# Performance work log

Measured on AMD Instinct MI355X. Metric: run time of the kernel, lower is better.

Reference implementation:

```python
import jax, jax.numpy as jnp
import numpy as np

B, F0, D = 4096, 39, 16
CIN = [128, 128, 128]


def setup_inputs() -> dict:
    key = jax.random.key(0)
    ks = jax.random.split(key, 4)
    x = jax.random.normal(ks[0], (B, F0, D), dtype=jnp.float32)
    fields = [F0] + CIN
    inp = {"embedded_features": x}
    for i in range(len(CIN)):
        cin = F0 * fields[i]
        cout = fields[i + 1]
        kw = jax.random.fold_in(ks[1], i)
        # Conv1d default init scale ~ 1/sqrt(fan_in)
        inp[f"W{i}"] = jax.random.normal(kw, (cout, cin), dtype=jnp.float32) / np.sqrt(cin)
        inp[f"b{i}"] = jnp.zeros((cout,), dtype=jnp.float32)
    return inp


def _cin_layer(X0, Xi, W, b):
    # Math identical to: outer_product [B,F0,Fi,D] -> reshape [B,F0*Fi,D] -> 1x1 Conv1d.
    # Conv1d(kernel=1) over the flattened F0*Fi channel dim is a contraction over (j,k):
    #   Xn[b,h,d] = sum_{j,k} W[h, j*Fi+k] * X0[b,j,d] * Xi[b,k,d] + b[h]
    H = W.shape[0]
    F0_, Fi = X0.shape[1], Xi.shape[1]
    Wr = W.reshape(H, F0_, Fi)
    return jnp.einsum('hjk,bjd,bkd->bhd', Wr, X0, Xi) + b[None, :, None]


def reference(embedded_features, W0, b0, W1, b1, W2, b2):
    X0 = embedded_features  # [B, F0, D]
    Ws = [(W0, b0), (W1, b1), (W2, b2)]
    Xi = X0
    res = []
    for W, b in Ws:
        Xi = _cin_layer(X0, Xi, W, b)  # [B, H_i, D]
        res.append(Xi.sum(axis=2))     # sum over embedding dim
    return jnp.concatenate(res, axis=1)  # [B, sum(cin_size)]
```

## Files before the change

### kernel.cpp

```cpp
#include <hip/hip_runtime.h>
#include <stdint.h>


#define NB_F0 39
#define NB_H  128
#define NB_B  4096

typedef float f32x4  __attribute__((ext_vector_type(4)));
typedef float f32x16 __attribute__((ext_vector_type(16)));
typedef short s16x8  __attribute__((ext_vector_type(8)));

__device__ __forceinline__ void dma16(const void* g, void* l) {
  __builtin_amdgcn_global_load_lds(
      (const __attribute__((address_space(1))) unsigned int*)g,
      (__attribute__((address_space(3))) unsigned int*)l, 16, 0, 0);
}

__device__ __forceinline__ unsigned short rne_bf16(float f) {
  union { float f; unsigned u; } v; v.f = f;
  return (unsigned short)((v.u + 0x7fffu + ((v.u >> 16) & 1u)) >> 16);
}
__device__ __forceinline__ float bf16_to_f32(unsigned short s) {
  union { unsigned u; float f; } v; v.u = ((unsigned)s) << 16;
  return v.f;
}

__global__ void prep_x0_kernel(const float* __restrict__ X0g,
                               unsigned short* __restrict__ X0T,
                               unsigned short* __restrict__ X0c) {
  const int b = blockIdx.x;
  const int t = threadIdx.x;
  {
    const int d  = t >> 4;
    const int k4 = (t & 15) << 2;
    unsigned short vv[4];
#pragma unroll
    for (int i = 0; i < 4; ++i) {
      const int k = k4 + i;
      vv[i] = (k < NB_F0) ? rne_bf16(X0g[(size_t)b * (NB_F0 * 16) + k * 16 + d])
                          : (unsigned short)0;
    }
    ushort4 pk; pk.x = vv[0]; pk.y = vv[1]; pk.z = vv[2]; pk.w = vv[3];
    *(ushort4*)&X0T[((size_t)b * 16 + d) * 64 + k4] = pk;
  }
  for (int idx = t; idx < NB_F0 * 16; idx += 256) {
    const int j = idx >> 4, pos = idx & 15;
    const int d = (pos & 3) | (((pos >> 3) & 1) << 2) | (((pos >> 2) & 1) << 3);
    X0c[(size_t)b * (NB_F0 * 16) + idx] =
        rne_bf16(X0g[(size_t)b * (NB_F0 * 16) + j * 16 + d]);
  }
}

__global__ void prep_w_kernel(const float* __restrict__ Wsrc,
                              unsigned short* __restrict__ Wdst,
                              int Fi, int kshift, int total) {
  int idx = blockIdx.x * 256 + threadIdx.x;
  if (idx >= total) return;
  const int i    = idx & 7;
  const int lane = (idx >> 3) & 63;
  const int c    = (idx >> 9) & ((1 << kshift) - 1);
  const int jt   = idx >> (9 + kshift);
  const int t    = jt & 3;
  const int j    = jt >> 2;
  const int h = t * 32 + (lane & 31);
  const int k = c * 16 + ((lane >> 5) << 3) + i;
  unsigned short v = 0;
  if (k < Fi) v = rne_bf16(Wsrc[(size_t)h * (NB_F0 * Fi) + j * Fi + k]);
  Wdst[idx] = v;
}

template <int FI_PAD, bool STORE_XN>
__global__ __launch_bounds__(256, 3) void cin_layer(
    const unsigned short* __restrict__ Wf,
    const unsigned short* __restrict__ XiT,
    const unsigned short* __restrict__ X0c,
    const float* __restrict__ bias,
    unsigned short* __restrict__ XnT,
    float* __restrict__ outp)
{
  constexpr int KPASS = FI_PAD / 64;
  constexpr int KC16  = FI_PAD / 16;
  constexpr int S     = NB_F0 * KPASS;

  __shared__ __attribute__((aligned(16))) unsigned short Wlds[2][2048];
  __shared__ __attribute__((aligned(16))) unsigned short x0s[16 * NB_F0 * 16];

  const int tid  = threadIdx.x;
  const int lane = tid & 63;
  const int wv   = tid >> 6;
  const int L    = lane >> 5;
  const int col  = lane & 31;
  const int ht   = blockIdx.x >> 8;
  const int bblk = (blockIdx.x & 255) * 16;
  const int bwave = bblk + wv * 4;

  auto dma_stage = [&](int s, int buf) {
    const int pass = (KPASS == 2 && s >= NB_F0) ? 1 : 0;
    const int j = s - pass * NB_F0;
    const unsigned short* src =
        Wf + (((size_t)(j * 4 + ht) * KC16) + pass * 4 + wv) * 512 + lane * 8;
    dma16(src, &Wlds[buf][wv * 512]);
  };

  {
    const unsigned short* src = X0c + (size_t)bblk * (NB_F0 * 16);
    for (int c = tid; c < (16 * NB_F0 * 16) / 8; c += 256)
      *(s16x8*)&x0s[c * 8] = *(const s16x8*)&src[c * 8];
  }
  dma_stage(0, 0);

  s16x8 af[2][4];
  auto load_af = [&](int pass) {
#pragma unroll
    for (int P = 0; P < 2; ++P) {
      const unsigned short* base = XiT +
          ((size_t)(bwave + 2 * P + (col >> 4)) * 16 + (col & 15)) * FI_PAD +
          pass * 64 + L * 8;
#pragma unroll
      for (int c = 0; c < 4; ++c) af[P][c] = *(const s16x8*)(base + c * 16);
    }
  };
  load_af(0);

  f32x16 Xacc[2], kZero;
#pragma unroll
  for (int r = 0; r < 16; ++r) { Xacc[0][r] = 0.f; Xacc[1][r] = 0.f; kZero[r] = 0.f; }

  const int x0base = (wv * 4) * (NB_F0 * 16) + L * 8;

  for (int s = 0; s < S; ++s) {
    __syncthreads();
    if (s + 1 < S) dma_stage(s + 1, (s + 1) & 1);
    if (KPASS == 2 && s == NB_F0) load_af(1);

    const int j = (KPASS == 2 && s >= NB_F0) ? s - NB_F0 : s;
    const unsigned short* wb = &Wlds[s & 1][lane * 8];
    const s16x8 w0 = *(const s16x8*)(wb);
    const s16x8 w1 = *(const s16x8*)(wb + 512);
    const s16x8 w2 = *(const s16x8*)(wb + 1024);
    const s16x8 w3 = *(const s16x8*)(wb + 1536);

    f32x16 y0, y1;
    y0 = __builtin_amdgcn_mfma_f32_32x32x16_bf16(af[0][0], w0, kZero, 0, 0, 0);
    y1 = __builtin_amdgcn_mfma_f32_32x32x16_bf16(af[1][0], w0, kZero, 0, 0, 0);
    y0 = __builtin_amdgcn_mfma_f32_32x32x16_bf16(af[0][1], w1, y0, 0, 0, 0);
    y1 = __builtin_amdgcn_mfma_f32_32x32x16_bf16(af[1][1], w1, y1, 0, 0, 0);
    y0 = __builtin_amdgcn_mfma_f32_32x32x16_bf16(af[0][2], w2, y0, 0, 0, 0);
    y1 = __builtin_amdgcn_mfma_f32_32x32x16_bf16(af[1][2], w2, y1, 0, 0, 0);
    y0 = __builtin_amdgcn_mfma_f32_32x32x16_bf16(af[0][3], w3, y0, 0, 0, 0);
    y1 = __builtin_amdgcn_mfma_f32_32x32x16_bf16(af[1][3], w3, y1, 0, 0, 0);

#pragma unroll
    for (int P = 0; P < 2; ++P) {
      const f32x16& y = (P == 0) ? y0 : y1;
#pragma unroll
      for (int bh = 0; bh < 2; ++bh) {
        const s16x8 xu = *(const s16x8*)
            &x0s[x0base + (2 * P + bh) * (NB_F0 * 16) + j * 16];
#pragma unroll
        for (int m = 0; m < 8; ++m)
          Xacc[P][bh * 8 + m] +=
              bf16_to_f32((unsigned short)xu[m]) * y[bh * 8 + m];
      }
    }
  }

  const float bias_v = bias[ht * 32 + col];
#pragma unroll
  for (int P = 0; P < 2; ++P) {
#pragma unroll
    for (int bh = 0; bh < 2; ++bh) {
      const int b = bwave + 2 * P + bh;
      float v[8];
#pragma unroll
      for (int m = 0; m < 8; ++m) v[m] = Xacc[P][bh * 8 + m] + bias_v;
      if (STORE_XN) {
#pragma unroll
        for (int m = 0; m < 8; ++m) {
          const int d = (m & 3) + 8 * ((m >> 2) & 1) + 4 * L;
          XnT[((size_t)b * 16 + d) * NB_H + ht * 32 + col] = rne_bf16(v[m]);
        }
      }
      float tot = ((v[0] + v[1]) + (v[2] + v[3])) + ((v[4] + v[5]) + (v[6] + v[7]));
      tot += __shfl_xor(tot, 32);
      if (lane < 32) outp[(size_t)b * 384 + ht * 32 + lane] = tot;
    }
  }
}

extern "C" void kernel_launch(void* const* d_in, const int* in_sizes, int n_in,
                              void* d_out, int out_size, void* d_ws, size_t ws_size,
                              hipStream_t stream) {
  (void)in_sizes; (void)n_in; (void)out_size; (void)ws_size;
  const float* X0g = (const float*)d_in[0];
  const float* W0  = (const float*)d_in[1];
  const float* b0  = (const float*)d_in[2];
  const float* W1  = (const float*)d_in[3];
  const float* b1  = (const float*)d_in[4];
  const float* W2  = (const float*)d_in[5];
  const float* b2  = (const float*)d_in[6];
  float* out = (float*)d_out;

  char* p = (char*)d_ws;
  unsigned short* X0T = (unsigned short*)p; p += (size_t)NB_B * 16 * 64 * 2;
  unsigned short* X0c = (unsigned short*)p; p += (size_t)NB_B * NB_F0 * 16 * 2;
  unsigned short* X1T = (unsigned short*)p; p += (size_t)NB_B * 16 * 128 * 2;
  unsigned short* X2T = (unsigned short*)p; p += (size_t)NB_B * 16 * 128 * 2;
  unsigned short* Wf0 = (unsigned short*)p; p += (size_t)NB_F0 * 4 * 4 * 512 * 2;
  unsigned short* Wf1 = (unsigned short*)p; p += (size_t)NB_F0 * 4 * 8 * 512 * 2;
  unsigned short* Wf2 = (unsigned short*)p; p += (size_t)NB_F0 * 4 * 8 * 512 * 2;

  hipLaunchKernelGGL(prep_x0_kernel, dim3(NB_B), dim3(256), 0, stream,
                     X0g, X0T, X0c);
  const int tw0  = NB_F0 * 4 * 4 * 512;
  const int tw12 = NB_F0 * 4 * 8 * 512;
  hipLaunchKernelGGL(prep_w_kernel, dim3((tw0 + 255) / 256), dim3(256), 0, stream,
                     W0, Wf0, 39, 2, tw0);
  hipLaunchKernelGGL(prep_w_kernel, dim3((tw12 + 255) / 256), dim3(256), 0, stream,
                     W1, Wf1, 128, 3, tw12);
  hipLaunchKernelGGL(prep_w_kernel, dim3((tw12 + 255) / 256), dim3(256), 0, stream,
                     W2, Wf2, 128, 3, tw12);

  hipLaunchKernelGGL((cin_layer<64, true>),   dim3(1024), dim3(256), 0, stream,
                     Wf0, X0T, X0c, b0, X1T, out + 0);
  hipLaunchKernelGGL((cin_layer<128, true>),  dim3(1024), dim3(256), 0, stream,
                     Wf1, X1T, X0c, b1, X2T, out + 128);
  hipLaunchKernelGGL((cin_layer<128, false>), dim3(1024), dim3(256), 0, stream,
                     Wf2, X2T, X0c, b2, (unsigned short*)nullptr, out + 256);
}
```

Baseline: 328.3 us.

## Double batch rows per block to reuse W tiles across more samples

Each block now covers 32 batch rows instead of 16, with each wave holding four A-fragment groups and four accumulators, so every DMA'd W tile feeds twice as many MFMAs and the grid is halved. The elementwise X0 scaling is rewritten as a vector FMA with a cheaper bf16 unpack. The cost is more registers and LDS per block, with launch bounds lowered to 2 blocks per SIMD and fewer blocks in flight.

```diff
diff --git a/kernel.cpp b/kernel.cpp
--- a/kernel.cpp
+++ b/kernel.cpp
@@ -70,7 +70,7 @@
 }
 
 template <int FI_PAD, bool STORE_XN>
-__global__ __launch_bounds__(256, 3) void cin_layer(
+__global__ __launch_bounds__(256, 2) void cin_layer(
     const unsigned short* __restrict__ Wf,
     const unsigned short* __restrict__ XiT,
     const unsigned short* __restrict__ X0c,
@@ -83,16 +83,16 @@
   constexpr int S     = NB_F0 * KPASS;
 
   __shared__ __attribute__((aligned(16))) unsigned short Wlds[2][2048];
-  __shared__ __attribute__((aligned(16))) unsigned short x0s[16 * NB_F0 * 16];
+  __shared__ __attribute__((aligned(16))) unsigned short x0s[32 * NB_F0 * 16];
 
   const int tid  = threadIdx.x;
   const int lane = tid & 63;
   const int wv   = tid >> 6;
   const int L    = lane >> 5;
   const int col  = lane & 31;
-  const int ht   = blockIdx.x >> 8;
-  const int bblk = (blockIdx.x & 255) * 16;
-  const int bwave = bblk + wv * 4;
+  const int ht   = blockIdx.x >> 7;
+  const int bblk = (blockIdx.x & 127) * 32;
+  const int bwave = bblk + wv * 8;
 
   auto dma_stage = [&](int s, int buf) {
     const int pass = (KPASS == 2 && s >= NB_F0) ? 1 : 0;
@@ -104,15 +104,15 @@
 
   {
     const unsigned short* src = X0c + (size_t)bblk * (NB_F0 * 16);
-    for (int c = tid; c < (16 * NB_F0 * 16) / 8; c += 256)
+    for (int c = tid; c < (32 * NB_F0 * 16) / 8; c += 256)
       *(s16x8*)&x0s[c * 8] = *(const s16x8*)&src[c * 8];
   }
   dma_stage(0, 0);
 
-  s16x8 af[2][4];
+  s16x8 af[4][4];
   auto load_af = [&](int pass) {
 #pragma unroll
-    for (int P = 0; P < 2; ++P) {
+    for (int P = 0; P < 4; ++P) {
       const unsigned short* base = XiT +
           ((size_t)(bwave + 2 * P + (col >> 4)) * 16 + (col & 15)) * FI_PAD +
           pass * 64 + L * 8;
@@ -122,11 +122,13 @@
   };
   load_af(0);
 
-  f32x16 Xacc[2], kZero;
-#pragma unroll
-  for (int r = 0; r < 16; ++r) { Xacc[0][r] = 0.f; Xacc[1][r] = 0.f; kZero[r] = 0.f; }
-
-  const int x0base = (wv * 4) * (NB_F0 * 16) + L * 8;
+  f32x16 Xacc[4], kZero;
+#pragma unroll
+  for (int r = 0; r < 16; ++r) kZero[r] = 0.f;
+#pragma unroll
+  for (int P = 0; P < 4; ++P) Xacc[P] = kZero;
+
+  const int x0base = (wv * 8) * (NB_F0 * 16) + L * 8;
 
   for (int s = 0; s < S; ++s) {
     __syncthreads();
@@ -140,34 +142,33 @@
     const s16x8 w2 = *(const s16x8*)(wb + 1024);
     const s16x8 w3 = *(const s16x8*)(wb + 1536);
 
-    f32x16 y0, y1;
-    y0 = __builtin_amdgcn_mfma_f32_32x32x16_bf16(af[0][0], w0, kZero, 0, 0, 0);
-    y1 = __builtin_amdgcn_mfma_f32_32x32x16_bf16(af[1][0], w0, kZero, 0, 0, 0);
-    y0 = __builtin_amdgcn_mfma_f32_32x32x16_bf16(af[0][1], w1, y0, 0, 0, 0);
-    y1 = __builtin_amdgcn_mfma_f32_32x32x16_bf16(af[1][1], w1, y1, 0, 0, 0);
-    y0 = __builtin_amdgcn_mfma_f32_32x32x16_bf16(af[0][2], w2, y0, 0, 0, 0);
-    y1 = __builtin_amdgcn_mfma_f32_32x32x16_bf16(af[1][2], w2, y1, 0, 0, 0);
-    y0 = __builtin_amdgcn_mfma_f32_32x32x16_bf16(af[0][3], w3, y0, 0, 0, 0);
-    y1 = __builtin_amdgcn_mfma_f32_32x32x16_bf16(af[1][3], w3, y1, 0, 0, 0);
-
-#pragma unroll
-    for (int P = 0; P < 2; ++P) {
-      const f32x16& y = (P == 0) ? y0 : y1;
-#pragma unroll
-      for (int bh = 0; bh < 2; ++bh) {
-        const s16x8 xu = *(const s16x8*)
-            &x0s[x0base + (2 * P + bh) * (NB_F0 * 16) + j * 16];
-#pragma unroll
-        for (int m = 0; m < 8; ++m)
-          Xacc[P][bh * 8 + m] +=
-              bf16_to_f32((unsigned short)xu[m]) * y[bh * 8 + m];
+#pragma unroll
+    for (int P = 0; P < 4; ++P) {
+      f32x16 y;
+      y = __builtin_amdgcn_mfma_f32_32x32x16_bf16(af[P][0], w0, kZero, 0, 0, 0);
+      y = __builtin_amdgcn_mfma_f32_32x32x16_bf16(af[P][1], w1, y, 0, 0, 0);
+      y = __builtin_amdgcn_mfma_f32_32x32x16_bf16(af[P][2], w2, y, 0, 0, 0);
+      y = __builtin_amdgcn_mfma_f32_32x32x16_bf16(af[P][3], w3, y, 0, 0, 0);
+
+      const uint4 xu0 = *(const uint4*)
+          &x0s[x0base + (2 * P + 0) * (NB_F0 * 16) + j * 16];
+      const uint4 xu1 = *(const uint4*)
+          &x0s[x0base + (2 * P + 1) * (NB_F0 * 16) + j * 16];
+      const unsigned wd[8] = {xu0.x, xu0.y, xu0.z, xu0.w,
+                              xu1.x, xu1.y, xu1.z, xu1.w};
+      f32x16 xsc;
+#pragma unroll
+      for (int i = 0; i < 8; ++i) {
+        xsc[2 * i]     = __uint_as_float(wd[i] << 16);
+        xsc[2 * i + 1] = __uint_as_float(wd[i] & 0xffff0000u);
       }
+      Xacc[P] = __builtin_elementwise_fma(xsc, y, Xacc[P]);
     }
   }
 
   const float bias_v = bias[ht * 32 + col];
 #pragma unroll
-  for (int P = 0; P < 2; ++P) {
+  for (int P = 0; P < 4; ++P) {
 #pragma unroll
     for (int bh = 0; bh < 2; ++bh) {
       const int b = bwave + 2 * P + bh;
@@ -221,10 +222,10 @@
   hipLaunchKernelGGL(prep_w_kernel, dim3((tw12 + 255) / 256), dim3(256), 0, stream,
                      W2, Wf2, 128, 3, tw12);
 
-  hipLaunchKernelGGL((cin_layer<64, true>),   dim3(1024), dim3(256), 0, stream,
+  hipLaunchKernelGGL((cin_layer<64, true>),   dim3(512), dim3(256), 0, stream,
                      Wf0, X0T, X0c, b0, X1T, out + 0);
-  hipLaunchKernelGGL((cin_layer<128, true>),  dim3(1024), dim3(256), 0, stream,
+  hipLaunchKernelGGL((cin_layer<128, true>),  dim3(512), dim3(256), 0, stream,
                      Wf1, X1T, X0c, b1, X2T, out + 128);
-  hipLaunchKernelGGL((cin_layer<128, false>), dim3(1024), dim3(256), 0, stream,
+  hipLaunchKernelGGL((cin_layer<128, false>), dim3(512), dim3(256), 0, stream,
                      Wf2, X2T, X0c, b2, (unsigned short*)nullptr, out + 256);
 }
```

New measurement: 316.3 us. 1.04x faster.
